# Optimization experiments

Measured on AMD Instinct MI355X. Metric: run time of the kernel, lower is better.

Reference implementation:

```python
import jax, jax.numpy as jnp
import numpy as np

N_NODES = 50000
N_EDGES = 800000
IN_F = 256
HID = 64
N_CLASSES = 32
LEAKY_SLOPE = 0.2


def _gat_layer(x, src, dst, W, a_src, a_dst):
    # Standard single-head GAT (GraphAttentionLayer_P0 semantics):
    # h = x W; e_ij = LeakyReLU(a_src.h_j + a_dst.h_i); softmax over in-edges of i;
    # out_i = sum_j alpha_ij h_j
    h = x @ W                                        # [N, F']
    alpha_s = h @ a_src                              # [N]
    alpha_d = h @ a_dst                              # [N]
    e = jax.nn.leaky_relu(alpha_s[src] + alpha_d[dst], LEAKY_SLOPE)  # [E]
    # segment softmax over edges grouped by destination node
    m = jax.ops.segment_max(e, dst, num_segments=N_NODES)           # [N]
    m = jnp.where(jnp.isfinite(m), m, 0.0)            # empty segments -> -inf
    ex = jnp.exp(e - m[dst])                          # [E]
    denom = jax.ops.segment_sum(ex, dst, num_segments=N_NODES)       # [N]
    denom = jnp.where(denom == 0.0, 1.0, denom)
    alpha = ex / denom[dst]                           # [E]
    out = jax.ops.segment_sum(alpha[:, None] * h[src], dst, num_segments=N_NODES)
    return out                                        # [N, F']


def setup_inputs() -> dict:
    key = jax.random.key(0)
    ks = jax.random.split(key, 8)
    x = jax.random.normal(ks[0], (N_NODES, IN_F), dtype=jnp.float32)
    edge_index = jax.random.randint(ks[1], (2, N_EDGES), 0, N_NODES, dtype=jnp.int64)
    s1 = 1.0 / np.sqrt(IN_F)
    s2 = 1.0 / np.sqrt(HID)
    W1 = jax.random.uniform(ks[2], (IN_F, HID), jnp.float32, -s1, s1)
    a1_src = jax.random.uniform(ks[3], (HID,), jnp.float32, -s2, s2)
    a1_dst = jax.random.uniform(ks[4], (HID,), jnp.float32, -s2, s2)
    W2 = jax.random.uniform(ks[5], (HID, N_CLASSES), jnp.float32, -s2, s2)
    s3 = 1.0 / np.sqrt(N_CLASSES)
    a2_src = jax.random.uniform(ks[6], (N_CLASSES,), jnp.float32, -s3, s3)
    a2_dst = jax.random.uniform(ks[7], (N_CLASSES,), jnp.float32, -s3, s3)
    return {"x": x, "edge_index": edge_index, "W1": W1, "a1_src": a1_src,
            "a1_dst": a1_dst, "W2": W2, "a2_src": a2_src, "a2_dst": a2_dst}


def reference(x, edge_index, W1, a1_src, a1_dst, W2, a2_src, a2_dst):
    src, dst = edge_index[0], edge_index[1]
    h = _gat_layer(x, src, dst, W1, a1_src, a1_dst)
    h = jax.nn.relu(h)
    out = _gat_layer(h, src, dst, W2, a2_src, a2_dst)
    return out
```

## Files before the change

### kernel.cpp

```cpp
#include <hip/hip_runtime.h>
#include <math.h>

#define NN 50000
#define NE 800000
#define INF_DIM 256
#define HIDF 64
#define NC 32
#define SLOPE 0.2f


__global__ void k_zero(int* __restrict__ counts){
  int i = blockIdx.x*blockDim.x + threadIdx.x;
  if(i < NN) counts[i] = 0;
}

__global__ void k_hist(const int* __restrict__ dst, int* __restrict__ counts){
  int e = blockIdx.x*blockDim.x + threadIdx.x;
  if(e < NE) atomicAdd(&counts[dst[e]], 1);
}

__global__ void k_scan_a(const int* __restrict__ counts, int* __restrict__ rowstart,
                         int* __restrict__ blocksums){
  __shared__ int wsum[4];
  int tid = threadIdx.x;
  int idx = blockIdx.x*1024 + tid*4;
  int v0 = (idx+0<NN)?counts[idx+0]:0;
  int v1 = (idx+1<NN)?counts[idx+1]:0;
  int v2 = (idx+2<NN)?counts[idx+2]:0;
  int v3 = (idx+3<NN)?counts[idx+3]:0;
  int s0=v0, s1=s0+v1, s2=s1+v2, s3=s2+v3;
  int lane = tid & 63, w = tid >> 6;
  int x = s3;
  #pragma unroll
  for(int off=1; off<64; off<<=1){
    int y = __shfl_up(x, off, 64);
    if(lane >= off) x += y;
  }
  if(lane==63) wsum[w] = x;
  __syncthreads();
  int woff = 0;
  for(int i=0;i<w;i++) woff += wsum[i];
  int excl = woff + (x - s3);
  if(idx+0<NN) rowstart[idx+1] = excl + s0;
  if(idx+1<NN) rowstart[idx+2] = excl + s1;
  if(idx+2<NN) rowstart[idx+3] = excl + s2;
  if(idx+3<NN) rowstart[idx+4] = excl + s3;
  if(tid==0) blocksums[blockIdx.x] = wsum[0]+wsum[1]+wsum[2]+wsum[3];
}

__global__ void k_scan_b(const int* __restrict__ blocksums, int* __restrict__ blockoff){
  int lane = threadIdx.x;
  const int nb = (NN + 1023)/1024;
  int v = (lane<nb)? blocksums[lane] : 0;
  int x = v;
  #pragma unroll
  for(int off=1; off<64; off<<=1){
    int y = __shfl_up(x, off, 64);
    if(lane >= off) x += y;
  }
  if(lane<nb) blockoff[lane] = x - v;
}

__global__ void k_scan_c(const int* __restrict__ counts, int* __restrict__ rowstart,
                         const int* __restrict__ blockoff, int* __restrict__ cursor){
  int i = blockIdx.x*blockDim.x + threadIdx.x;
  if(i < NN){
    int incl = rowstart[i+1] + blockoff[i>>10];
    rowstart[i+1] = incl;
    cursor[i] = incl - counts[i];
    if(i==0) rowstart[0] = 0;
  }
}

__global__ void k_scatter(const int* __restrict__ src, const int* __restrict__ dst,
                          int* __restrict__ cursor, int* __restrict__ ssrc){
  int e = blockIdx.x*blockDim.x + threadIdx.x;
  if(e < NE){
    int d = dst[e];
    int pos = atomicAdd(&cursor[d], 1);
    ssrc[pos] = src[e];
  }
}


__global__ __launch_bounds__(64) void k_gemm1(
    const float* __restrict__ x, const float* __restrict__ W,
    const float* __restrict__ a_s, const float* __restrict__ a_d,
    float* __restrict__ h, float* __restrict__ as_o, float* __restrict__ ad_o){
  int lane = threadIdx.x;
  int n = blockIdx.x*64 + lane;
  int nr = (n < NN) ? n : (NN-1);
  const float* xrow = x + (size_t)nr*INF_DIM;
  const float4* Wv = reinterpret_cast<const float4*>(W);

  float4 acc[16];
  #pragma unroll
  for(int i=0;i<16;i++) acc[i] = make_float4(0.f,0.f,0.f,0.f);

  float4 xc[4], xn[4];
  #pragma unroll
  for(int j=0;j<4;j++) xc[j] = *reinterpret_cast<const float4*>(xrow + j*4);

  for(int kt=0; kt<16; ++kt){
    if(kt < 15){
      #pragma unroll
      for(int j=0;j<4;j++)
        xn[j] = *reinterpret_cast<const float4*>(xrow + (kt+1)*16 + j*4);
    }
    #pragma unroll
    for(int k4=0;k4<4;k4++){
      int kbase = kt*16 + k4*4;
      float4 xk = xc[k4];
      #pragma unroll
      for(int cb=0;cb<16;cb++){
        float4 w0 = Wv[(kbase+0)*16 + cb];
        float4 w1 = Wv[(kbase+1)*16 + cb];
        float4 w2 = Wv[(kbase+2)*16 + cb];
        float4 w3 = Wv[(kbase+3)*16 + cb];
        acc[cb].x += xk.x*w0.x + xk.y*w1.x + xk.z*w2.x + xk.w*w3.x;
        acc[cb].y += xk.x*w0.y + xk.y*w1.y + xk.z*w2.y + xk.w*w3.y;
        acc[cb].z += xk.x*w0.z + xk.y*w1.z + xk.z*w2.z + xk.w*w3.z;
        acc[cb].w += xk.x*w0.w + xk.y*w1.w + xk.z*w2.w + xk.w*w3.w;
      }
    }
    #pragma unroll
    for(int j=0;j<4;j++) xc[j] = xn[j];
  }

  const float4* asv = reinterpret_cast<const float4*>(a_s);
  const float4* adv = reinterpret_cast<const float4*>(a_d);
  float sv = 0.f, dv = 0.f;
  #pragma unroll
  for(int cb=0;cb<16;cb++){
    float4 a4 = asv[cb], d4 = adv[cb];
    sv += acc[cb].x*a4.x + acc[cb].y*a4.y + acc[cb].z*a4.z + acc[cb].w*a4.w;
    dv += acc[cb].x*d4.x + acc[cb].y*d4.y + acc[cb].z*d4.z + acc[cb].w*d4.w;
  }
  if(n < NN){
    #pragma unroll
    for(int cb=0;cb<16;cb++)
      *reinterpret_cast<float4*>(h + (size_t)n*HIDF + cb*4) = acc[cb];
    as_o[n] = sv; ad_o[n] = dv;
  }
}


__global__ __launch_bounds__(256) void k_agg1(
    const float* __restrict__ h1, const float* __restrict__ as1, const float* __restrict__ ad1,
    const int* __restrict__ rowstart, const int* __restrict__ ssrc,
    float* __restrict__ r1){
  __shared__ int2 sp[4][64];
  int wv = threadIdx.x >> 6;
  int lane = threadIdx.x & 63;
  int n = blockIdx.x*4 + wv;
  int rs = rowstart[n], re = rowstart[n+1];
  float adn = ad1[n];
  float m = -1e30f, l = 0.f, acc = 0.f;
  for(int base=rs; base<re; base+=64){
    int cnt = re - base; if(cnt > 64) cnt = 64;
    int s = 0; float z = -1e30f;
    if(lane < cnt){
      s = ssrc[base+lane];
      float zz = as1[s] + adn;
      z = zz > 0.f ? zz : SLOPE*zz;
    }
    float cm = z;
    #pragma unroll
    for(int off=32; off>=1; off>>=1) cm = fmaxf(cm, __shfl_xor(cm, off, 64));
    float nm = fmaxf(m, cm);
    float sc = __expf(m - nm);
    float p = (lane<cnt) ? __expf(z - nm) : 0.f;
    float cs = p;
    #pragma unroll
    for(int off=32; off>=1; off>>=1) cs += __shfl_xor(cs, off, 64);
    l = l*sc + cs;
    acc *= sc;
    sp[wv][lane] = make_int2(s, __float_as_int(p));
    for(int e=0; e<cnt; ++e){
      int2 v = sp[wv][e];
      acc += __int_as_float(v.y) * h1[(size_t)v.x*HIDF + lane];
    }
    m = nm;
  }
  float o = (l > 0.f) ? acc/l : 0.f;
  r1[(size_t)n*HIDF + lane] = fmaxf(o, 0.f);
}


__global__ __launch_bounds__(64) void k_gemm2(
    const float* __restrict__ r1, const float* __restrict__ W2,
    const float* __restrict__ a_s, const float* __restrict__ a_d,
    float* __restrict__ h2, float* __restrict__ as_o, float* __restrict__ ad_o){
  int lane = threadIdx.x;
  int n = blockIdx.x*64 + lane;
  int nr = (n < NN) ? n : (NN-1);
  const float* xrow = r1 + (size_t)nr*HIDF;
  const float4* Wv = reinterpret_cast<const float4*>(W2);

  float4 acc[8];
  #pragma unroll
  for(int i=0;i<8;i++) acc[i] = make_float4(0.f,0.f,0.f,0.f);

  float4 xc[4], xn[4];
  #pragma unroll
  for(int j=0;j<4;j++) xc[j] = *reinterpret_cast<const float4*>(xrow + j*4);

  for(int kt=0; kt<4; ++kt){
    if(kt < 3){
      #pragma unroll
      for(int j=0;j<4;j++)
        xn[j] = *reinterpret_cast<const float4*>(xrow + (kt+1)*16 + j*4);
    }
    #pragma unroll
    for(int k4=0;k4<4;k4++){
      int kbase = kt*16 + k4*4;
      float4 xk = xc[k4];
      #pragma unroll
      for(int cb=0;cb<8;cb++){
        float4 w0 = Wv[(kbase+0)*8 + cb];
        float4 w1 = Wv[(kbase+1)*8 + cb];
        float4 w2 = Wv[(kbase+2)*8 + cb];
        float4 w3 = Wv[(kbase+3)*8 + cb];
        acc[cb].x += xk.x*w0.x + xk.y*w1.x + xk.z*w2.x + xk.w*w3.x;
        acc[cb].y += xk.x*w0.y + xk.y*w1.y + xk.z*w2.y + xk.w*w3.y;
        acc[cb].z += xk.x*w0.z + xk.y*w1.z + xk.z*w2.z + xk.w*w3.z;
        acc[cb].w += xk.x*w0.w + xk.y*w1.w + xk.z*w2.w + xk.w*w3.w;
      }
    }
    #pragma unroll
    for(int j=0;j<4;j++) xc[j] = xn[j];
  }

  const float4* asv = reinterpret_cast<const float4*>(a_s);
  const float4* adv = reinterpret_cast<const float4*>(a_d);
  float sv = 0.f, dv = 0.f;
  #pragma unroll
  for(int cb=0;cb<8;cb++){
    float4 a4 = asv[cb], d4 = adv[cb];
    sv += acc[cb].x*a4.x + acc[cb].y*a4.y + acc[cb].z*a4.z + acc[cb].w*a4.w;
    dv += acc[cb].x*d4.x + acc[cb].y*d4.y + acc[cb].z*d4.z + acc[cb].w*d4.w;
  }
  if(n < NN){
    #pragma unroll
    for(int cb=0;cb<8;cb++)
      *reinterpret_cast<float4*>(h2 + (size_t)n*NC + cb*4) = acc[cb];
    as_o[n] = sv; ad_o[n] = dv;
  }
}


__global__ __launch_bounds__(256) void k_agg2(
    const float* __restrict__ h2, const float* __restrict__ as2, const float* __restrict__ ad2,
    const int* __restrict__ rowstart, const int* __restrict__ ssrc,
    float* __restrict__ out){
  __shared__ int2 sp2[8][32];
  int tid = threadIdx.x;
  int sub = tid >> 5;
  int c = tid & 31;
  int n = blockIdx.x*8 + sub;
  int rs = rowstart[n], re = rowstart[n+1];
  float adn = ad2[n];
  float m = -1e30f, l = 0.f, acc = 0.f;
  for(int base=rs; base<re; base+=32){
    int cnt = re - base; if(cnt > 32) cnt = 32;
    int s = 0; float z = -1e30f;
    if(c < cnt){
      s = ssrc[base+c];
      float zz = as2[s] + adn;
      z = zz > 0.f ? zz : SLOPE*zz;
    }
    float cm = z;
    #pragma unroll
    for(int off=16; off>=1; off>>=1) cm = fmaxf(cm, __shfl_xor(cm, off, 32));
    float nm = fmaxf(m, cm);
    float sc = __expf(m - nm);
    float p = (c<cnt) ? __expf(z - nm) : 0.f;
    float cs = p;
    #pragma unroll
    for(int off=16; off>=1; off>>=1) cs += __shfl_xor(cs, off, 32);
    l = l*sc + cs;
    acc *= sc;
    sp2[sub][c] = make_int2(s, __float_as_int(p));
    for(int e=0; e<cnt; ++e){
      int2 v = sp2[sub][e];
      acc += __int_as_float(v.y) * h2[(size_t)v.x*NC + c];
    }
    m = nm;
  }
  out[(size_t)n*NC + c] = (l > 0.f) ? acc/l : 0.f;
}


extern "C" void kernel_launch(void* const* d_in, const int* in_sizes, int n_in,
                              void* d_out, int out_size, void* d_ws, size_t ws_size,
                              hipStream_t stream){
  const float* x   = (const float*)d_in[0];
  const int*   ei  = (const int*)d_in[1];
  const float* W1  = (const float*)d_in[2];
  const float* a1s = (const float*)d_in[3];
  const float* a1d = (const float*)d_in[4];
  const float* W2  = (const float*)d_in[5];
  const float* a2s = (const float*)d_in[6];
  const float* a2d = (const float*)d_in[7];
  const int* srcIdx = ei;
  const int* dstIdx = ei + NE;
  float* out = (float*)d_out;

  char* wsp = (char*)d_ws;
  size_t off = 0;
  auto alloc = [&](size_t bytes)->void*{
    void* p = wsp + off;
    off = (off + bytes + 255) & ~(size_t)255;
    return p;
  };
  int* counts    = (int*)alloc((size_t)NN*sizeof(int));
  int* rowstart  = (int*)alloc((size_t)(NN+1)*sizeof(int));
  int* cursor    = (int*)alloc((size_t)NN*sizeof(int));
  int* blocksums = (int*)alloc(64*sizeof(int));
  int* blockoff  = (int*)alloc(64*sizeof(int));
  int* ssrc      = (int*)alloc((size_t)NE*sizeof(int));
  float* h1      = (float*)alloc((size_t)NN*HIDF*sizeof(float));
  float* as1     = (float*)alloc((size_t)NN*sizeof(float));
  float* ad1     = (float*)alloc((size_t)NN*sizeof(float));
  float* r1      = (float*)alloc((size_t)NN*HIDF*sizeof(float));
  float* h2  = h1;
  float* as2 = as1;
  float* ad2 = ad1;

  k_zero   <<<(NN+255)/256, 256, 0, stream>>>(counts);
  k_hist   <<<(NE+255)/256, 256, 0, stream>>>(dstIdx, counts);
  k_scan_a <<<(NN+1023)/1024, 256, 0, stream>>>(counts, rowstart, blocksums);
  k_scan_b <<<1, 64, 0, stream>>>(blocksums, blockoff);
  k_scan_c <<<(NN+255)/256, 256, 0, stream>>>(counts, rowstart, blockoff, cursor);
  k_scatter<<<(NE+255)/256, 256, 0, stream>>>(srcIdx, dstIdx, cursor, ssrc);

  k_gemm1<<<(NN+63)/64, 64, 0, stream>>>(x, W1, a1s, a1d, h1, as1, ad1);
  k_agg1 <<<NN/4, 256, 0, stream>>>(h1, as1, ad1, rowstart, ssrc, r1);

  k_gemm2<<<(NN+63)/64, 64, 0, stream>>>(r1, W2, a2s, a2d, h2, as2, ad2);
  k_agg2 <<<NN/8, 256, 0, stream>>>(h2, as2, ad2, rowstart, ssrc, out);
}
```

Baseline: 351.5 us.

## Retile GEMMs with shared-memory weights and use shuffles in aggregation loops

Both projection GEMMs are retiled so each 64-thread block handles 32 nodes, with 8 threads per node, each owning a column slice. Weight tiles are staged in LDS, and the attention dot products are reduced with xor shuffles. This replaces per-thread scans over all output columns, which needed 64 accumulators and many redundant global weight loads. The aggregation kernels also drop their LDS staging of (src, p) pairs in favour of lane broadcasts via __shfl, unrolled by four to put more gathers in flight. The cost is more block-level syncs per K step in gemm1 and partially uncoalesced x row loads.

```diff
diff --git a/kernel.cpp b/kernel.cpp
--- a/kernel.cpp
+++ b/kernel.cpp
@@ -87,60 +87,80 @@
     const float* __restrict__ x, const float* __restrict__ W,
     const float* __restrict__ a_s, const float* __restrict__ a_d,
     float* __restrict__ h, float* __restrict__ as_o, float* __restrict__ ad_o){
-  int lane = threadIdx.x;
-  int n = blockIdx.x*64 + lane;
-  int nr = (n < NN) ? n : (NN-1);
-  const float* xrow = x + (size_t)nr*INF_DIM;
+  __shared__ float ws[8*64];
+  float4* wsv = reinterpret_cast<float4*>(ws);
   const float4* Wv = reinterpret_cast<const float4*>(W);
-
-  float4 acc[16];
-  #pragma unroll
-  for(int i=0;i<16;i++) acc[i] = make_float4(0.f,0.f,0.f,0.f);
-
-  float4 xc[4], xn[4];
-  #pragma unroll
-  for(int j=0;j<4;j++) xc[j] = *reinterpret_cast<const float4*>(xrow + j*4);
-
-  for(int kt=0; kt<16; ++kt){
-    if(kt < 15){
+  int tid = threadIdx.x;
+  int ng = tid >> 3, cg = tid & 7;
+  int nb0 = blockIdx.x*32;
+
+  const float* xrow[4];
+  #pragma unroll
+  for(int i=0;i<4;i++){
+    int n = nb0 + ng + 8*i;
+    xrow[i] = x + (size_t)((n < NN) ? n : (NN-1))*INF_DIM;
+  }
+
+  float4 acc[4][2];
+  #pragma unroll
+  for(int i=0;i<4;i++){ acc[i][0]=make_float4(0.f,0.f,0.f,0.f); acc[i][1]=make_float4(0.f,0.f,0.f,0.f); }
+
+  for(int st=0; st<32; ++st){
+    int k0 = st*8;
+    wsv[tid]      = Wv[k0*16 + tid];
+    wsv[tid + 64] = Wv[k0*16 + 64 + tid];
+    float4 xa[4][2];
+    #pragma unroll
+    for(int i=0;i<4;i++){
+      xa[i][0] = *reinterpret_cast<const float4*>(xrow[i] + k0);
+      xa[i][1] = *reinterpret_cast<const float4*>(xrow[i] + k0 + 4);
+    }
+    __syncthreads();
+    #pragma unroll
+    for(int k4=0;k4<2;k4++){
+      float4 wf[4][2];
       #pragma unroll
-      for(int j=0;j<4;j++)
-        xn[j] = *reinterpret_cast<const float4*>(xrow + (kt+1)*16 + j*4);
-    }
-    #pragma unroll
-    for(int k4=0;k4<4;k4++){
-      int kbase = kt*16 + k4*4;
-      float4 xk = xc[k4];
+      for(int kk=0;kk<4;kk++){
+        wf[kk][0] = wsv[(k4*4+kk)*16 + cg*2];
+        wf[kk][1] = wsv[(k4*4+kk)*16 + cg*2 + 1];
+      }
       #pragma unroll
-      for(int cb=0;cb<16;cb++){
-        float4 w0 = Wv[(kbase+0)*16 + cb];
-        float4 w1 = Wv[(kbase+1)*16 + cb];
-        float4 w2 = Wv[(kbase+2)*16 + cb];
-        float4 w3 = Wv[(kbase+3)*16 + cb];
-        acc[cb].x += xk.x*w0.x + xk.y*w1.x + xk.z*w2.x + xk.w*w3.x;
-        acc[cb].y += xk.x*w0.y + xk.y*w1.y + xk.z*w2.y + xk.w*w3.y;
-        acc[cb].z += xk.x*w0.z + xk.y*w1.z + xk.z*w2.z + xk.w*w3.z;
-        acc[cb].w += xk.x*w0.w + xk.y*w1.w + xk.z*w2.w + xk.w*w3.w;
+      for(int i=0;i<4;i++){
+        float4 xv = xa[i][k4];
+        acc[i][0].x += xv.x*wf[0][0].x + xv.y*wf[1][0].x + xv.z*wf[2][0].x + xv.w*wf[3][0].x;
+        acc[i][0].y += xv.x*wf[0][0].y + xv.y*wf[1][0].y + xv.z*wf[2][0].y + xv.w*wf[3][0].y;
+        acc[i][0].z += xv.x*wf[0][0].z + xv.y*wf[1][0].z + xv.z*wf[2][0].z + xv.w*wf[3][0].z;
+        acc[i][0].w += xv.x*wf[0][0].w + xv.y*wf[1][0].w + xv.z*wf[2][0].w + xv.w*wf[3][0].w;
+        acc[i][1].x += xv.x*wf[0][1].x + xv.y*wf[1][1].x + xv.z*wf[2][1].x + xv.w*wf[3][1].x;
+        acc[i][1].y += xv.x*wf[0][1].y + xv.y*wf[1][1].y + xv.z*wf[2][1].y + xv.w*wf[3][1].y;
+        acc[i][1].z += xv.x*wf[0][1].z + xv.y*wf[1][1].z + xv.z*wf[2][1].z + xv.w*wf[3][1].z;
+        acc[i][1].w += xv.x*wf[0][1].w + xv.y*wf[1][1].w + xv.z*wf[2][1].w + xv.w*wf[3][1].w;
       }
     }
-    #pragma unroll
-    for(int j=0;j<4;j++) xc[j] = xn[j];
+    __syncthreads();
   }
 
   const float4* asv = reinterpret_cast<const float4*>(a_s);
   const float4* adv = reinterpret_cast<const float4*>(a_d);
-  float sv = 0.f, dv = 0.f;
-  #pragma unroll
-  for(int cb=0;cb<16;cb++){
-    float4 a4 = asv[cb], d4 = adv[cb];
-    sv += acc[cb].x*a4.x + acc[cb].y*a4.y + acc[cb].z*a4.z + acc[cb].w*a4.w;
-    dv += acc[cb].x*d4.x + acc[cb].y*d4.y + acc[cb].z*d4.z + acc[cb].w*d4.w;
-  }
-  if(n < NN){
-    #pragma unroll
-    for(int cb=0;cb<16;cb++)
-      *reinterpret_cast<float4*>(h + (size_t)n*HIDF + cb*4) = acc[cb];
-    as_o[n] = sv; ad_o[n] = dv;
+  float4 asA = asv[cg*2], asB = asv[cg*2+1];
+  float4 adA = adv[cg*2], adB = adv[cg*2+1];
+  #pragma unroll
+  for(int i=0;i<4;i++){
+    int n = nb0 + ng + 8*i;
+    float sv = acc[i][0].x*asA.x + acc[i][0].y*asA.y + acc[i][0].z*asA.z + acc[i][0].w*asA.w
+             + acc[i][1].x*asB.x + acc[i][1].y*asB.y + acc[i][1].z*asB.z + acc[i][1].w*asB.w;
+    float dv = acc[i][0].x*adA.x + acc[i][0].y*adA.y + acc[i][0].z*adA.z + acc[i][0].w*adA.w
+             + acc[i][1].x*adB.x + acc[i][1].y*adB.y + acc[i][1].z*adB.z + acc[i][1].w*adB.w;
+    #pragma unroll
+    for(int mk=1; mk<8; mk<<=1){
+      sv += __shfl_xor(sv, mk, 64);
+      dv += __shfl_xor(dv, mk, 64);
+    }
+    if(n < NN){
+      *reinterpret_cast<float4*>(h + (size_t)n*HIDF + cg*8)     = acc[i][0];
+      *reinterpret_cast<float4*>(h + (size_t)n*HIDF + cg*8 + 4) = acc[i][1];
+      if(cg==0){ as_o[n]=sv; ad_o[n]=dv; }
+    }
   }
 }
 
@@ -149,10 +169,8 @@
     const float* __restrict__ h1, const float* __restrict__ as1, const float* __restrict__ ad1,
     const int* __restrict__ rowstart, const int* __restrict__ ssrc,
     float* __restrict__ r1){
-  __shared__ int2 sp[4][64];
-  int wv = threadIdx.x >> 6;
   int lane = threadIdx.x & 63;
-  int n = blockIdx.x*4 + wv;
+  int n = blockIdx.x*4 + (threadIdx.x >> 6);
   int rs = rowstart[n], re = rowstart[n+1];
   float adn = ad1[n];
   float m = -1e30f, l = 0.f, acc = 0.f;
@@ -175,10 +193,22 @@
     for(int off=32; off>=1; off>>=1) cs += __shfl_xor(cs, off, 64);
     l = l*sc + cs;
     acc *= sc;
-    sp[wv][lane] = make_int2(s, __float_as_int(p));
-    for(int e=0; e<cnt; ++e){
-      int2 v = sp[wv][e];
-      acc += __int_as_float(v.y) * h1[(size_t)v.x*HIDF + lane];
+    int e = 0;
+    for(; e+4<=cnt; e+=4){
+      int   se0 = __shfl(s, e,   64), se1 = __shfl(s, e+1, 64);
+      int   se2 = __shfl(s, e+2, 64), se3 = __shfl(s, e+3, 64);
+      float pe0 = __shfl(p, e,   64), pe1 = __shfl(p, e+1, 64);
+      float pe2 = __shfl(p, e+2, 64), pe3 = __shfl(p, e+3, 64);
+      float v0 = h1[(size_t)se0*HIDF + lane];
+      float v1 = h1[(size_t)se1*HIDF + lane];
+      float v2 = h1[(size_t)se2*HIDF + lane];
+      float v3 = h1[(size_t)se3*HIDF + lane];
+      acc += pe0*v0; acc += pe1*v1; acc += pe2*v2; acc += pe3*v3;
+    }
+    for(; e<cnt; ++e){
+      int   se = __shfl(s, e, 64);
+      float pe = __shfl(p, e, 64);
+      acc += pe * h1[(size_t)se*HIDF + lane];
     }
     m = nm;
   }
@@ -191,60 +221,67 @@
     const float* __restrict__ r1, const float* __restrict__ W2,
     const float* __restrict__ a_s, const float* __restrict__ a_d,
     float* __restrict__ h2, float* __restrict__ as_o, float* __restrict__ ad_o){
-  int lane = threadIdx.x;
-  int n = blockIdx.x*64 + lane;
-  int nr = (n < NN) ? n : (NN-1);
-  const float* xrow = r1 + (size_t)nr*HIDF;
+  __shared__ float ws2[64*32];
+  float4* wsv = reinterpret_cast<float4*>(ws2);
   const float4* Wv = reinterpret_cast<const float4*>(W2);
-
-  float4 acc[8];
-  #pragma unroll
-  for(int i=0;i<8;i++) acc[i] = make_float4(0.f,0.f,0.f,0.f);
-
-  float4 xc[4], xn[4];
-  #pragma unroll
-  for(int j=0;j<4;j++) xc[j] = *reinterpret_cast<const float4*>(xrow + j*4);
-
-  for(int kt=0; kt<4; ++kt){
-    if(kt < 3){
+  int tid = threadIdx.x;
+  int ng = tid >> 3, cg = tid & 7;
+  int nb0 = blockIdx.x*32;
+  #pragma unroll
+  for(int j=0;j<8;j++) wsv[j*64 + tid] = Wv[j*64 + tid];
+
+  const float* xrow[4];
+  #pragma unroll
+  for(int i=0;i<4;i++){
+    int n = nb0 + ng + 8*i;
+    xrow[i] = r1 + (size_t)((n < NN) ? n : (NN-1))*HIDF;
+  }
+  float4 acc[4];
+  #pragma unroll
+  for(int i=0;i<4;i++) acc[i] = make_float4(0.f,0.f,0.f,0.f);
+  __syncthreads();
+
+  for(int st=0; st<8; ++st){
+    int k0 = st*8;
+    float4 xa[4][2];
+    #pragma unroll
+    for(int i=0;i<4;i++){
+      xa[i][0] = *reinterpret_cast<const float4*>(xrow[i] + k0);
+      xa[i][1] = *reinterpret_cast<const float4*>(xrow[i] + k0 + 4);
+    }
+    #pragma unroll
+    for(int k4=0;k4<2;k4++){
+      float4 wf[4];
       #pragma unroll
-      for(int j=0;j<4;j++)
-        xn[j] = *reinterpret_cast<const float4*>(xrow + (kt+1)*16 + j*4);
-    }
-    #pragma unroll
-    for(int k4=0;k4<4;k4++){
-      int kbase = kt*16 + k4*4;
-      float4 xk = xc[k4];
+      for(int kk=0;kk<4;kk++) wf[kk] = wsv[(k0 + k4*4 + kk)*8 + cg];
       #pragma unroll
-      for(int cb=0;cb<8;cb++){
-        float4 w0 = Wv[(kbase+0)*8 + cb];
-        float4 w1 = Wv[(kbase+1)*8 + cb];
-        float4 w2 = Wv[(kbase+2)*8 + cb];
-        float4 w3 = Wv[(kbase+3)*8 + cb];
-        acc[cb].x += xk.x*w0.x + xk.y*w1.x + xk.z*w2.x + xk.w*w3.x;
-        acc[cb].y += xk.x*w0.y + xk.y*w1.y + xk.z*w2.y + xk.w*w3.y;
-        acc[cb].z += xk.x*w0.z + xk.y*w1.z + xk.z*w2.z + xk.w*w3.z;
-        acc[cb].w += xk.x*w0.w + xk.y*w1.w + xk.z*w2.w + xk.w*w3.w;
+      for(int i=0;i<4;i++){
+        float4 xv = xa[i][k4];
+        acc[i].x += xv.x*wf[0].x + xv.y*wf[1].x + xv.z*wf[2].x + xv.w*wf[3].x;
+        acc[i].y += xv.x*wf[0].y + xv.y*wf[1].y + xv.z*wf[2].y + xv.w*wf[3].y;
+        acc[i].z += xv.x*wf[0].z + xv.y*wf[1].z + xv.z*wf[2].z + xv.w*wf[3].z;
+        acc[i].w += xv.x*wf[0].w + xv.y*wf[1].w + xv.z*wf[2].w + xv.w*wf[3].w;
       }
     }
-    #pragma unroll
-    for(int j=0;j<4;j++) xc[j] = xn[j];
   }
 
   const float4* asv = reinterpret_cast<const float4*>(a_s);
   const float4* adv = reinterpret_cast<const float4*>(a_d);
-  float sv = 0.f, dv = 0.f;
-  #pragma unroll
-  for(int cb=0;cb<8;cb++){
-    float4 a4 = asv[cb], d4 = adv[cb];
-    sv += acc[cb].x*a4.x + acc[cb].y*a4.y + acc[cb].z*a4.z + acc[cb].w*a4.w;
-    dv += acc[cb].x*d4.x + acc[cb].y*d4.y + acc[cb].z*d4.z + acc[cb].w*d4.w;
-  }
-  if(n < NN){
-    #pragma unroll
-    for(int cb=0;cb<8;cb++)
-      *reinterpret_cast<float4*>(h2 + (size_t)n*NC + cb*4) = acc[cb];
-    as_o[n] = sv; ad_o[n] = dv;
+  float4 as4 = asv[cg], ad4 = adv[cg];
+  #pragma unroll
+  for(int i=0;i<4;i++){
+    int n = nb0 + ng + 8*i;
+    float sv = acc[i].x*as4.x + acc[i].y*as4.y + acc[i].z*as4.z + acc[i].w*as4.w;
+    float dv = acc[i].x*ad4.x + acc[i].y*ad4.y + acc[i].z*ad4.z + acc[i].w*ad4.w;
+    #pragma unroll
+    for(int mk=1; mk<8; mk<<=1){
+      sv += __shfl_xor(sv, mk, 64);
+      dv += __shfl_xor(dv, mk, 64);
+    }
+    if(n < NN){
+      *reinterpret_cast<float4*>(h2 + (size_t)n*NC + cg*4) = acc[i];
+      if(cg==0){ as_o[n]=sv; ad_o[n]=dv; }
+    }
   }
 }
 
@@ -253,11 +290,9 @@
     const float* __restrict__ h2, const float* __restrict__ as2, const float* __restrict__ ad2,
     const int* __restrict__ rowstart, const int* __restrict__ ssrc,
     float* __restrict__ out){
-  __shared__ int2 sp2[8][32];
   int tid = threadIdx.x;
-  int sub = tid >> 5;
   int c = tid & 31;
-  int n = blockIdx.x*8 + sub;
+  int n = blockIdx.x*8 + (tid >> 5);
   int rs = rowstart[n], re = rowstart[n+1];
   float adn = ad2[n];
   float m = -1e30f, l = 0.f, acc = 0.f;
@@ -280,10 +315,22 @@
     for(int off=16; off>=1; off>>=1) cs += __shfl_xor(cs, off, 32);
     l = l*sc + cs;
     acc *= sc;
-    sp2[sub][c] = make_int2(s, __float_as_int(p));
-    for(int e=0; e<cnt; ++e){
-      int2 v = sp2[sub][e];
-      acc += __int_as_float(v.y) * h2[(size_t)v.x*NC + c];
+    int e = 0;
+    for(; e+4<=cnt; e+=4){
+      int   se0 = __shfl(s, e,   32), se1 = __shfl(s, e+1, 32);
+      int   se2 = __shfl(s, e+2, 32), se3 = __shfl(s, e+3, 32);
+      float pe0 = __shfl(p, e,   32), pe1 = __shfl(p, e+1, 32);
+      float pe2 = __shfl(p, e+2, 32), pe3 = __shfl(p, e+3, 32);
+      float v0 = h2[(size_t)se0*NC + c];
+      float v1 = h2[(size_t)se1*NC + c];
+      float v2 = h2[(size_t)se2*NC + c];
+      float v3 = h2[(size_t)se3*NC + c];
+      acc += pe0*v0; acc += pe1*v1; acc += pe2*v2; acc += pe3*v3;
+    }
+    for(; e<cnt; ++e){
+      int   se = __shfl(s, e, 32);
+      float pe = __shfl(p, e, 32);
+      acc += pe * h2[(size_t)se*NC + c];
     }
     m = nm;
   }
@@ -334,9 +381,9 @@
   k_scan_c <<<(NN+255)/256, 256, 0, stream>>>(counts, rowstart, blockoff, cursor);
   k_scatter<<<(NE+255)/256, 256, 0, stream>>>(srcIdx, dstIdx, cursor, ssrc);
 
-  k_gemm1<<<(NN+63)/64, 64, 0, stream>>>(x, W1, a1s, a1d, h1, as1, ad1);
+  k_gemm1<<<(NN+31)/32, 64, 0, stream>>>(x, W1, a1s, a1d, h1, as1, ad1);
   k_agg1 <<<NN/4, 256, 0, stream>>>(h1, as1, ad1, rowstart, ssrc, r1);
 
-  k_gemm2<<<(NN+63)/64, 64, 0, stream>>>(r1, W2, a2s, a2d, h2, as2, ad2);
+  k_gemm2<<<(NN+31)/32, 64, 0, stream>>>(r1, W2, a2s, a2d, h2, as2, ad2);
   k_agg2 <<<NN/8, 256, 0, stream>>>(h2, as2, ad2, rowstart, ssrc, out);
 }
```

Measured after the change: 302.7 us. 1.16x faster.
